# Optimization experiments

Hardware: AMD Instinct MI355X
Metric: run time of the kernel (lower is better)

## Reference

```python
import jax, jax.numpy as jnp
import numpy as np

# irrep blocks for 0e+1o+2e: dims 1, 3, 5 (total D=9)
BLOCKS = [(0, 1), (1, 4), (4, 9)]

def block_linear(x, W):
    # x: [N, C, 9], W: [3, C, C] -- e3nn Linear mixes channels within each irrep block
    outs = [jnp.einsum('ncd,cq->nqd', x[..., s:e], W[l]) for l, (s, e) in enumerate(BLOCKS)]
    return jnp.concatenate(outs, axis=-1)

def setup_inputs() -> dict:
    key = jax.random.key(0)
    ks = jax.random.split(key, 14)
    N, E, C, D, B, H, Z = 16384, 262144, 32, 9, 8, 64, 4
    inp = {
        'node_feats': jax.random.normal(ks[0], (N, C, D), jnp.float32),
        'node_attrs': jax.random.uniform(ks[1], (N, Z), jnp.float32),
        'edge_feats': jax.random.normal(ks[2], (E, B), jnp.float32),
        'edge_sh': jax.random.normal(ks[3], (E, D), jnp.float32),
        'cutoff': jax.random.uniform(ks[4], (E, 1), jnp.float32),
        # learned params
        'W_up': jax.random.normal(ks[5], (3, C, C), jnp.float32) / np.float32(np.sqrt(C)),
        'W1': jax.random.normal(ks[6], (B, H), jnp.float32) / np.float32(np.sqrt(B)),
        'W2': jax.random.normal(ks[7], (H, H), jnp.float32) / np.float32(np.sqrt(H)),
        'W3': jax.random.normal(ks[8], (H, C), jnp.float32) / np.float32(np.sqrt(H)),
        'W_lin': jax.random.normal(ks[9], (3, C, C), jnp.float32) / np.float32(np.sqrt(C)),
        'W_sc': jax.random.normal(ks[10], (Z, 3, C, C), jnp.float32) / np.float32(np.sqrt(C)),
        # fixed Clebsch-Gordan-like coupling tensor (constant structure of the TP)
        'CG': jax.random.normal(ks[11], (D, D, D), jnp.float32) / np.float32(D),
        'edge_src': jax.random.randint(ks[12], (E,), 0, N, jnp.int32),
        'edge_dst': jax.random.randint(ks[13], (E,), 0, N, jnp.int32),
    }
    return inp

def reference(node_feats, node_attrs, edge_feats, edge_sh, cutoff,
              W_up, W1, W2, W3, W_lin, W_sc, CG, edge_src, edge_dst):
    N = node_feats.shape[0]
    avg_num_neighbors = 16.0
    # linear_up: per-irrep channel mixing
    x = block_linear(node_feats, W_up)
    # radial MLP -> per-edge tensor-product weights, gated by cutoff
    h = jax.nn.silu(edge_feats @ W1)
    h = jax.nn.silu(h @ W2)
    w = (h @ W3) * cutoff  # [E, C]
    # gather source node feats, weighted equivariant tensor product per edge
    xs = x[edge_src]  # [E, C, D]
    m_ij = jnp.einsum('eci,ej,ijk,ec->eck', xs, edge_sh, CG, w)  # [E, C, D]
    # scatter-sum aggregation into destination nodes
    m_i = jax.ops.segment_sum(m_ij, edge_dst, num_segments=N)  # [N, C, D]
    # output linear + neighbor normalization
    m_i = block_linear(m_i, W_lin) / avg_num_neighbors
    # element-dependent self-connection from current message
    W_node = jnp.einsum('nz,zlcq->nlcq', node_attrs, W_sc)  # [N, 3, C, C]
    scs = jnp.concatenate(
        [jnp.einsum('ncd,ncq->nqd', m_i[..., s:e], W_node[:, l]) for l, (s, e) in enumerate(BLOCKS)],
        axis=-1)
    return (m_i, scs)
```

## Files before the change

### kernel.cpp

```cpp
#include <hip/hip_runtime.h>
#include <cstdint>

#define CC 32
#define DD 9
#define CD 288
#define BB 8
#define HH 64
#define ZZ 4
#define NB 8

typedef __attribute__((ext_vector_type(8))) short bf16x8;
typedef __attribute__((ext_vector_type(4))) float f32x4;
typedef __attribute__((ext_vector_type(2))) float f32x2;

__device__ __forceinline__ float silu_f(float v) {
  return v / (1.0f + __expf(-v));
}

__device__ __forceinline__ int blk_of(int d) { return d == 0 ? 0 : (d < 4 ? 1 : 2); }

__device__ __forceinline__ unsigned int f2bf(float f) {
  unsigned int u = __float_as_uint(f);
  return (u + 0x7fffu + ((u >> 16) & 1u)) >> 16;
}
__device__ __forceinline__ float bf_lo(unsigned int u) { return __uint_as_float(u << 16); }
__device__ __forceinline__ float bf_hi(unsigned int u) { return __uint_as_float(u & 0xffff0000u); }

__global__ __launch_bounds__(256) void k_zero(float* __restrict__ p, int n) {
  int i = blockIdx.x * 256 + threadIdx.x;
  if (i < n) p[i] = 0.0f;
}

__global__ __launch_bounds__(256) void k_hist(const int* __restrict__ edst,
                                              int* __restrict__ deg, int E) {
  int e = blockIdx.x * 256 + threadIdx.x;
  if (e < E) atomicAdd(&deg[edst[e]], 1);
}

__global__ __launch_bounds__(1024) void k_scan(const int* __restrict__ deg,
                                               int* __restrict__ offs,
                                               int* __restrict__ cursor, int N) {
  __shared__ int part[1024];
  int t = threadIdx.x;
  int chunk = (N + 1023) >> 10;
  int base = t * chunk;
  int lim = N - base; if (lim > chunk) lim = chunk; if (lim < 0) lim = 0;
  int s = 0;
  for (int i = 0; i < lim; ++i) s += deg[base + i];
  part[t] = s;
  __syncthreads();
  for (int off = 1; off < 1024; off <<= 1) {
    int v = part[t];
    int u = (t >= off) ? part[t - off] : 0;
    __syncthreads();
    part[t] = v + u;
    __syncthreads();
  }
  int run = (t == 0) ? 0 : part[t - 1];
  for (int i = 0; i < lim; ++i) {
    offs[base + i] = run;
    cursor[base + i] = run;
    run += deg[base + i];
  }
  if (t == 1023) offs[N] = run;
}

__global__ __launch_bounds__(256) void k_scatter(const int* __restrict__ edst,
                                                 const int* __restrict__ esrc,
                                                 const float* __restrict__ esh,
                                                 int* __restrict__ cursor,
                                                 int* __restrict__ eidx,
                                                 int* __restrict__ srcs,
                                                 unsigned int* __restrict__ esh_p, int E) {
  int e = blockIdx.x * 256 + threadIdx.x;
  if (e < E) {
    int d = edst[e];
    int pos = atomicAdd(&cursor[d], 1);
    eidx[pos] = e;
    srcs[pos] = esrc[e];
    const float* sp = esh + (size_t)e * 9;
    unsigned int* op = esh_p + (size_t)pos * 5;
#pragma unroll
    for (int jj = 0; jj < 5; ++jj) {
      unsigned int lo = f2bf(sp[2 * jj]);
      unsigned int hi = (jj < 4) ? f2bf(sp[2 * jj + 1]) : 0u;
      op[jj] = lo | (hi << 16);
    }
  }
}

__global__ __launch_bounds__(288, 1) void k_linear_up(
    const float* __restrict__ nf, const float* __restrict__ Wup,
    unsigned int* __restrict__ x_p, int N) {
  __shared__ float snf[NB][DD * 36];
  __shared__ float sval[NB][DD][CC];
  int t = threadIdx.x;
  int g = t >> 5, q = t & 31;
  int tc = t / 9, td = t - tc * 9;
  int l0 = blk_of(g);
  float wcol[CC];
#pragma unroll
  for (int c = 0; c < CC; ++c) wcol[c] = Wup[l0 * 1024 + c * 32 + q];
  int nbat = (N + NB - 1) / NB;
  int b = blockIdx.x;
  float r[NB];
  if (b < nbat) {
#pragma unroll
    for (int nb = 0; nb < NB; ++nb) {
      int n = b * NB + nb; if (n >= N) n = N - 1;
      r[nb] = nf[(size_t)n * CD + t];
    }
  }
  for (; b < nbat; b += gridDim.x) {
    int n0 = b * NB;
    __syncthreads();
#pragma unroll
    for (int nb = 0; nb < NB; ++nb) snf[nb][td * 36 + tc] = r[nb];
    __syncthreads();
    int b2 = b + gridDim.x;
    if (b2 < nbat) {
#pragma unroll
      for (int nb = 0; nb < NB; ++nb) {
        int n = b2 * NB + nb; if (n >= N) n = N - 1;
        r[nb] = nf[(size_t)n * CD + t];
      }
    }
#pragma unroll
    for (int nb = 0; nb < NB; ++nb) {
      const float4* rowp = (const float4*)(snf[nb] + g * 36);
      float a0 = 0.f, a1 = 0.f;
#pragma unroll
      for (int c4 = 0; c4 < 8; ++c4) {
        float4 bb = rowp[c4];
        a0 += bb.x * wcol[c4 * 4 + 0] + bb.y * wcol[c4 * 4 + 1];
        a1 += bb.z * wcol[c4 * 4 + 2] + bb.w * wcol[c4 * 4 + 3];
      }
      sval[nb][g][q] = a0 + a1;
    }
    __syncthreads();
#pragma unroll
    for (int it = 0; it < 5; ++it) {
      int idx = it * 288 + t;
      if (idx < NB * 160) {
        int nb = idx / 160, rr = idx - nb * 160;
        int p = rr >> 5, c = rr & 31;
        if (n0 + nb < N) {
          unsigned int lo = f2bf(sval[nb][2 * p][c]);
          unsigned int hi = (p < 4) ? f2bf(sval[nb][2 * p + 1][c]) : 0u;
          x_p[(size_t)(n0 + nb) * 160 + rr] = lo | (hi << 16);
        }
      }
    }
  }
}

__global__ __launch_bounds__(64) void k_mlp_mfma(
    const float* __restrict__ ef, const float* __restrict__ cut,
    const float* __restrict__ W1, const float* __restrict__ W2,
    const float* __restrict__ W3, const int* __restrict__ eidx,
    unsigned int* __restrict__ w_p, int E) {
  __shared__ ushort buf[4096];
  __shared__ float scut[64];
  int l = threadIdx.x;
  int h = l >> 4, li = l & 15;
  bf16x8 A2[4][2];
#pragma unroll
  for (int qm = 0; qm < 4; ++qm)
#pragma unroll
    for (int kb = 0; kb < 2; ++kb)
#pragma unroll
      for (int j = 0; j < 8; ++j)
        A2[qm][kb][j] = (short)f2bf(W2[(32 * kb + 8 * h + j) * HH + 16 * qm + li]);
  bf16x8 A3[2][2];
#pragma unroll
  for (int cm = 0; cm < 2; ++cm)
#pragma unroll
    for (int kb = 0; kb < 2; ++kb)
#pragma unroll
      for (int j = 0; j < 8; ++j)
        A3[cm][kb][j] = (short)f2bf(W3[(32 * kb + 8 * h + j) * CC + 16 * cm + li]);

  int ntile = E >> 6;
  for (int tile = blockIdx.x; tile < ntile; tile += gridDim.x) {
    int pos = tile * 64 + l;
    int eo = eidx[pos];
    const float4* efp = (const float4*)(ef + (size_t)eo * BB);
    float4 efa = efp[0];
    float4 efb = efp[1];
    scut[l] = cut[eo];
    float efv[BB] = {efa.x, efa.y, efa.z, efa.w, efb.x, efb.y, efb.z, efb.w};
#pragma unroll
    for (int g = 0; g < 8; ++g) {
      float hv[8];
#pragma unroll
      for (int jj = 0; jj < 8; ++jj) {
        int q = g * 8 + jj;
        float a = 0.f;
#pragma unroll
        for (int kin = 0; kin < BB; ++kin) a += efv[kin] * W1[kin * HH + q];
        hv[jj] = silu_f(a);
      }
      unsigned int d0 = f2bf(hv[0]) | (f2bf(hv[1]) << 16);
      unsigned int d1 = f2bf(hv[2]) | (f2bf(hv[3]) << 16);
      unsigned int d2 = f2bf(hv[4]) | (f2bf(hv[5]) << 16);
      unsigned int d3 = f2bf(hv[6]) | (f2bf(hv[7]) << 16);
      int F = ((l >> 4) * 2 + (g >> 2)) * 4 + (g & 3);
      *(uint4*)&buf[(F * 16 + li) * 8] = make_uint4(d0, d1, d2, d3);
    }
    f32x4 acc2[4][4];
#pragma unroll
    for (int qm = 0; qm < 4; ++qm)
#pragma unroll
      for (int nb = 0; nb < 4; ++nb) acc2[qm][nb] = (f32x4){0.f, 0.f, 0.f, 0.f};
#pragma unroll
    for (int nb = 0; nb < 4; ++nb)
#pragma unroll
      for (int kb = 0; kb < 2; ++kb) {
        int F = (nb * 2 + kb) * 4 + h;
        bf16x8 Bf = *(const bf16x8*)&buf[(F * 16 + li) * 8];
#pragma unroll
        for (int qm = 0; qm < 4; ++qm)
          acc2[qm][nb] = __builtin_amdgcn_mfma_f32_16x16x32_bf16(
              A2[qm][kb], Bf, acc2[qm][nb], 0, 0, 0);
      }
#pragma unroll
    for (int qm = 0; qm < 4; ++qm)
#pragma unroll
      for (int nb = 0; nb < 4; ++nb) {
        float v0 = silu_f(acc2[qm][nb][0]);
        float v1 = silu_f(acc2[qm][nb][1]);
        float v2 = silu_f(acc2[qm][nb][2]);
        float v3 = silu_f(acc2[qm][nb][3]);
        unsigned int lo = f2bf(v0) | (f2bf(v1) << 16);
        unsigned int hi = f2bf(v2) | (f2bf(v3) << 16);
        int G = (nb * 2 + (qm >> 1)) * 4 + ((2 * qm + (h >> 1)) & 3);
        *(uint2*)&buf[(G * 16 + li) * 8 + (h & 1) * 4] = make_uint2(lo, hi);
      }
    f32x4 acc3[2][4];
#pragma unroll
    for (int cm = 0; cm < 2; ++cm)
#pragma unroll
      for (int nb = 0; nb < 4; ++nb) acc3[cm][nb] = (f32x4){0.f, 0.f, 0.f, 0.f};
#pragma unroll
    for (int nb = 0; nb < 4; ++nb)
#pragma unroll
      for (int kb = 0; kb < 2; ++kb) {
        int G = (nb * 2 + kb) * 4 + h;
        bf16x8 Bf = *(const bf16x8*)&buf[(G * 16 + li) * 8];
#pragma unroll
        for (int cm = 0; cm < 2; ++cm)
          acc3[cm][nb] = __builtin_amdgcn_mfma_f32_16x16x32_bf16(
              A3[cm][kb], Bf, acc3[cm][nb], 0, 0, 0);
      }
#pragma unroll
    for (int nb = 0; nb < 4; ++nb) {
      float cv = scut[16 * nb + li];
#pragma unroll
      for (int cm = 0; cm < 2; ++cm) {
        unsigned int lo = f2bf(acc3[cm][nb][0] * cv) | (f2bf(acc3[cm][nb][1] * cv) << 16);
        unsigned int hi = f2bf(acc3[cm][nb][2] * cv) | (f2bf(acc3[cm][nb][3] * cv) << 16);
        *(uint2*)&w_p[(size_t)(tile * 64 + 16 * nb + li) * 16 + 8 * cm + 2 * h] =
            make_uint2(lo, hi);
      }
    }
  }
}

__global__ __launch_bounds__(256) void k_gather(
    const unsigned int* __restrict__ x_p, const unsigned int* __restrict__ w_p,
    const unsigned int* __restrict__ esh_p, const float* __restrict__ CG,
    const int* __restrict__ offs, const int* __restrict__ srcs,
    float* __restrict__ mpre, int N) {
  int wid = (blockIdx.x * 256 + threadIdx.x) >> 6;
  if (wid >= N) return;
  int lane = threadIdx.x & 63;
  int h = lane >> 5, c = lane & 31;
  int beg = offs[wid], end = offs[wid + 1];
  f32x2 Pp[36];
  float P8[9];
#pragma unroll
  for (int i = 0; i < 36; ++i) Pp[i] = (f32x2){0.f, 0.f};
#pragma unroll
  for (int i = 0; i < 9; ++i) P8[i] = 0.f;

  bool okc;
  unsigned int wu_c;
  unsigned int shd_c[5];
  unsigned int xd_c[5];
  {
    int p = beg + h;
    okc = p < end;
    int pp = okc ? p : beg;
    int s = srcs[pp];
    wu_c = w_p[(size_t)pp * 16 + (c >> 1)];
    const unsigned int* shp = esh_p + (size_t)pp * 5;
#pragma unroll
    for (int j = 0; j < 5; ++j) shd_c[j] = shp[j];
    const unsigned int* xp = x_p + (size_t)s * 160 + c;
    xd_c[0] = xp[0]; xd_c[1] = xp[32]; xd_c[2] = xp[64]; xd_c[3] = xp[96]; xd_c[4] = xp[128];
  }

  for (int p0 = beg; p0 < end; p0 += 2) {
    int pn = p0 + 2 + h;
    bool okn = pn < end;
    int ppn = okn ? pn : beg;
    int s_n = srcs[ppn];
    unsigned int wu_n = w_p[(size_t)ppn * 16 + (c >> 1)];
    unsigned int shd_n[5];
    {
      const unsigned int* shp = esh_p + (size_t)ppn * 5;
#pragma unroll
      for (int j = 0; j < 5; ++j) shd_n[j] = shp[j];
    }
    unsigned int xd_n[5];
    {
      const unsigned int* xp = x_p + (size_t)s_n * 160 + c;
      xd_n[0] = xp[0]; xd_n[1] = xp[32]; xd_n[2] = xp[64]; xd_n[3] = xp[96]; xd_n[4] = xp[128];
    }
    float wc = okc ? ((c & 1) ? bf_hi(wu_c) : bf_lo(wu_c)) : 0.f;
    f32x2 sh2[4];
    sh2[0] = (f32x2){bf_lo(shd_c[0]), bf_hi(shd_c[0])};
    sh2[1] = (f32x2){bf_lo(shd_c[1]), bf_hi(shd_c[1])};
    sh2[2] = (f32x2){bf_lo(shd_c[2]), bf_hi(shd_c[2])};
    sh2[3] = (f32x2){bf_lo(shd_c[3]), bf_hi(shd_c[3])};
    float sh8 = bf_lo(shd_c[4]);
    float xs[DD];
    xs[0] = bf_lo(xd_c[0]); xs[1] = bf_hi(xd_c[0]);
    xs[2] = bf_lo(xd_c[1]); xs[3] = bf_hi(xd_c[1]);
    xs[4] = bf_lo(xd_c[2]); xs[5] = bf_hi(xd_c[2]);
    xs[6] = bf_lo(xd_c[3]); xs[7] = bf_hi(xd_c[3]);
    xs[8] = bf_lo(xd_c[4]);
#pragma unroll
    for (int i = 0; i < DD; ++i) {
      float t = wc * xs[i];
      f32x2 t2 = (f32x2){t, t};
#pragma unroll
      for (int jp = 0; jp < 4; ++jp) Pp[i * 4 + jp] = t2 * sh2[jp] + Pp[i * 4 + jp];
      P8[i] += t * sh8;
    }
    okc = okn;
    wu_c = wu_n;
#pragma unroll
    for (int j = 0; j < 5; ++j) { shd_c[j] = shd_n[j]; xd_c[j] = xd_n[j]; }
  }

  f32x2 m2[4];
  float m8 = 0.f;
#pragma unroll
  for (int kp = 0; kp < 4; ++kp) m2[kp] = (f32x2){0.f, 0.f};
#pragma unroll
  for (int i = 0; i < DD; ++i) {
#pragma unroll
    for (int j = 0; j < DD; ++j) {
      float p = (j < 8) ? ((j & 1) ? Pp[i * 4 + (j >> 1)].y : Pp[i * 4 + (j >> 1)].x)
                        : P8[i];
      f32x2 p2 = (f32x2){p, p};
      const float* cgr = CG + i * 81 + j * DD;
#pragma unroll
      for (int kp = 0; kp < 4; ++kp) {
        f32x2 cg2 = (f32x2){cgr[2 * kp], cgr[2 * kp + 1]};
        m2[kp] = p2 * cg2 + m2[kp];
      }
      m8 += p * cgr[8];
    }
  }
  float m[DD];
  m[0] = m2[0].x; m[1] = m2[0].y;
  m[2] = m2[1].x; m[3] = m2[1].y;
  m[4] = m2[2].x; m[5] = m2[2].y;
  m[6] = m2[3].x; m[7] = m2[3].y;
  m[8] = m8;
#pragma unroll
  for (int k = 0; k < DD; ++k) m[k] += __shfl_xor(m[k], 32);
  if (h == 0) {
    float* mp = mpre + (size_t)wid * CD + c;
#pragma unroll
    for (int k = 0; k < DD; ++k) mp[k * 32] = m[k];
  }
}

__global__ __launch_bounds__(288, 1) void k_out(
    const float* __restrict__ attrs, const float* __restrict__ Wlin,
    const float* __restrict__ Wsc,
    float* __restrict__ out1, float* __restrict__ out2, int N) {
  __shared__ float smp[NB][CD];
  __shared__ float smt[NB][CD];
  __shared__ float sres1[NB * CD];
  __shared__ float sres2[NB * CD];
  int t = threadIdx.x;
  int g = t >> 5, q = t & 31;
  int l0 = blk_of(g);
  float wl[CC];
#pragma unroll
  for (int c = 0; c < CC; ++c) wl[c] = Wlin[l0 * 1024 + c * 32 + q];
  float ws0[CC], ws1[CC], ws2[CC], ws3[CC];
#pragma unroll
  for (int c = 0; c < CC; ++c) {
    ws0[c] = Wsc[0 * 3072 + l0 * 1024 + c * 32 + q];
    ws1[c] = Wsc[1 * 3072 + l0 * 1024 + c * 32 + q];
    ws2[c] = Wsc[2 * 3072 + l0 * 1024 + c * 32 + q];
    ws3[c] = Wsc[3 * 3072 + l0 * 1024 + c * 32 + q];
  }
  int nbat = (N + NB - 1) / NB;
  int b = blockIdx.x;
  float r[NB];
  if (b < nbat) {
#pragma unroll
    for (int nb = 0; nb < NB; ++nb) r[nb] = out2[(size_t)(b * NB + nb) * CD + t];
  }
  for (; b < nbat; b += gridDim.x) {
    int n0 = b * NB;
    __syncthreads();
#pragma unroll
    for (int nb = 0; nb < NB; ++nb) smp[nb][t] = r[nb];
    float4 av[NB];
#pragma unroll
    for (int nb = 0; nb < NB; ++nb) av[nb] = ((const float4*)attrs)[n0 + nb];
    __syncthreads();
    int b2 = b + gridDim.x;
    if (b2 < nbat) {
#pragma unroll
      for (int nb = 0; nb < NB; ++nb) r[nb] = out2[(size_t)(b2 * NB + nb) * CD + t];
    }
#pragma unroll
    for (int nb = 0; nb < NB; ++nb) {
      const float4* rowp = (const float4*)(smp[nb] + g * 32);
      float b0 = 0.f, b1 = 0.f;
#pragma unroll
      for (int c4 = 0; c4 < 8; ++c4) {
        float4 bb = rowp[c4];
        b0 += bb.x * wl[c4 * 4 + 0] + bb.y * wl[c4 * 4 + 1];
        b1 += bb.z * wl[c4 * 4 + 2] + bb.w * wl[c4 * 4 + 3];
      }
      float v = (b0 + b1) * (1.0f / 16.0f);
      smt[nb][t] = v;
      sres1[nb * CD + q * DD + g] = v;
    }
    __syncthreads();
#pragma unroll
    for (int nb = 0; nb < NB; ++nb) {
      const float4* rowp = (const float4*)(smt[nb] + g * 32);
      float z0 = 0.f, z1 = 0.f, z2 = 0.f, z3 = 0.f;
#pragma unroll
      for (int c4 = 0; c4 < 8; ++c4) {
        float4 bb = rowp[c4];
#pragma unroll
        for (int j = 0; j < 4; ++j) {
          float bv = (j == 0) ? bb.x : (j == 1) ? bb.y : (j == 2) ? bb.z : bb.w;
          int c = c4 * 4 + j;
          z0 += bv * ws0[c];
          z1 += bv * ws1[c];
          z2 += bv * ws2[c];
          z3 += bv * ws3[c];
        }
      }
      float4 a = av[nb];
      sres2[nb * CD + q * DD + g] = a.x * z0 + a.y * z1 + a.z * z2 + a.w * z3;
    }
    __syncthreads();
#pragma unroll
    for (int rr = 0; rr < (NB * 72) / 288; ++rr) {
      int s = rr * 288 + t;
      int nb = s / 72, idx = s - nb * 72;
      ((float4*)(out1 + (size_t)(n0 + nb) * CD))[idx] = ((const float4*)sres1)[s];
      ((float4*)(out2 + (size_t)(n0 + nb) * CD))[idx] = ((const float4*)sres2)[s];
    }
  }
}

extern "C" void kernel_launch(void* const* d_in, const int* in_sizes, int n_in,
                              void* d_out, int out_size, void* d_ws, size_t ws_size,
                              hipStream_t stream) {
  const float* nf    = (const float*)d_in[0];
  const float* attrs = (const float*)d_in[1];
  const float* ef    = (const float*)d_in[2];
  const float* esh   = (const float*)d_in[3];
  const float* cutv  = (const float*)d_in[4];
  const float* Wup   = (const float*)d_in[5];
  const float* W1    = (const float*)d_in[6];
  const float* W2    = (const float*)d_in[7];
  const float* W3    = (const float*)d_in[8];
  const float* Wlin  = (const float*)d_in[9];
  const float* Wsc   = (const float*)d_in[10];
  const float* CG    = (const float*)d_in[11];
  const int* esrc    = (const int*)d_in[12];
  const int* edst    = (const int*)d_in[13];
  int N = in_sizes[0] / CD;
  int E = in_sizes[12];
  float* out1 = (float*)d_out;
  float* out2 = out1 + (size_t)N * CD;

  unsigned int* x_p   = (unsigned int*)d_ws;
  unsigned int* w_p   = x_p + (size_t)N * 160;
  unsigned int* esh_p = w_p + (size_t)E * 16;
  int* deg     = (int*)(esh_p + (size_t)E * 5);
  int* offs    = deg + N;
  int* cursor  = offs + N + 1;
  int* eidx    = cursor + N;
  int* srcs    = eidx + E;

  k_zero<<<(N + 255) / 256, 256, 0, stream>>>((float*)deg, N);
  k_hist<<<(E + 255) / 256, 256, 0, stream>>>(edst, deg, E);
  k_scan<<<1, 1024, 0, stream>>>(deg, offs, cursor, N);
  k_scatter<<<(E + 255) / 256, 256, 0, stream>>>(edst, esrc, esh, cursor, eidx, srcs, esh_p, E);
  k_linear_up<<<512, 288, 0, stream>>>(nf, Wup, x_p, N);
  k_mlp_mfma<<<4096, 64, 0, stream>>>(ef, cutv, W1, W2, W3, eidx, w_p, E);
  k_gather<<<(N + 3) / 4, 256, 0, stream>>>(x_p, w_p, esh_p, CG, offs, srcs, out2, N);
  k_out<<<512, 288, 0, stream>>>(attrs, Wlin, Wsc, out1, out2, N);
}
```

Baseline: 236.5 us.

## Make gather kernel persistent with atomic work-stealing and cross-node prefetch

The gather kernel now launches a fixed grid of 2048 blocks. Each wavefront takes destination nodes from a global atomic counter, which is reset inside the scan kernel, instead of being given one node per wave. While it finishes the CG contraction for the current node, each wave prefetches the first edge data for the next node, so the load latency at node boundaries overlaps with compute. The aim is better load balance across nodes with uneven degree and fewer wave launch overheads. The cost is one atomic per node and a serialized dependency on the counter.

Result: slower. 478.8 us (+102.5%).

```diff
diff --git a/kernel.cpp b/kernel.cpp
--- a/kernel.cpp
+++ b/kernel.cpp
@@ -39,9 +39,11 @@
 
 __global__ __launch_bounds__(1024) void k_scan(const int* __restrict__ deg,
                                                int* __restrict__ offs,
-                                               int* __restrict__ cursor, int N) {
+                                               int* __restrict__ cursor,
+                                               int* __restrict__ wctr, int N) {
   __shared__ int part[1024];
   int t = threadIdx.x;
+  if (t == 0) wctr[0] = 0;
   int chunk = (N + 1023) >> 10;
   int base = t * chunk;
   int lim = N - base; if (lim > chunk) lim = chunk; if (lim < 0) lim = 0;
@@ -270,18 +272,18 @@
     const unsigned int* __restrict__ x_p, const unsigned int* __restrict__ w_p,
     const unsigned int* __restrict__ esh_p, const float* __restrict__ CG,
     const int* __restrict__ offs, const int* __restrict__ srcs,
-    float* __restrict__ mpre, int N) {
-  int wid = (blockIdx.x * 256 + threadIdx.x) >> 6;
-  if (wid >= N) return;
+    int* __restrict__ wctr, float* __restrict__ mpre, int N) {
   int lane = threadIdx.x & 63;
   int h = lane >> 5, c = lane & 31;
-  int beg = offs[wid], end = offs[wid + 1];
-  f32x2 Pp[36];
-  float P8[9];
-#pragma unroll
-  for (int i = 0; i < 36; ++i) Pp[i] = (f32x2){0.f, 0.f};
-#pragma unroll
-  for (int i = 0; i < 9; ++i) P8[i] = 0.f;
+
+  int cur;
+  {
+    int v = 0;
+    if (lane == 0) v = atomicAdd(wctr, 1);
+    cur = __shfl(v, 0, 64);
+  }
+  if (cur >= N) return;
+  int beg = offs[cur], end = offs[cur + 1];
 
   bool okc;
   unsigned int wu_c;
@@ -300,82 +302,116 @@
     xd_c[0] = xp[0]; xd_c[1] = xp[32]; xd_c[2] = xp[64]; xd_c[3] = xp[96]; xd_c[4] = xp[128];
   }
 
-  for (int p0 = beg; p0 < end; p0 += 2) {
-    int pn = p0 + 2 + h;
-    bool okn = pn < end;
-    int ppn = okn ? pn : beg;
-    int s_n = srcs[ppn];
-    unsigned int wu_n = w_p[(size_t)ppn * 16 + (c >> 1)];
-    unsigned int shd_n[5];
+  while (true) {
+    f32x2 Pp[36];
+    float P8[9];
+#pragma unroll
+    for (int i = 0; i < 36; ++i) Pp[i] = (f32x2){0.f, 0.f};
+#pragma unroll
+    for (int i = 0; i < 9; ++i) P8[i] = 0.f;
+
+    for (int p0 = beg; p0 < end; p0 += 2) {
+      int pn = p0 + 2 + h;
+      bool okn = pn < end;
+      int ppn = okn ? pn : beg;
+      int s_n = srcs[ppn];
+      unsigned int wu_n = w_p[(size_t)ppn * 16 + (c >> 1)];
+      unsigned int shd_n[5];
+      {
+        const unsigned int* shp = esh_p + (size_t)ppn * 5;
+#pragma unroll
+        for (int j = 0; j < 5; ++j) shd_n[j] = shp[j];
+      }
+      unsigned int xd_n[5];
+      {
+        const unsigned int* xp = x_p + (size_t)s_n * 160 + c;
+        xd_n[0] = xp[0]; xd_n[1] = xp[32]; xd_n[2] = xp[64]; xd_n[3] = xp[96]; xd_n[4] = xp[128];
+      }
+      float wc = okc ? ((c & 1) ? bf_hi(wu_c) : bf_lo(wu_c)) : 0.f;
+      f32x2 sh2[4];
+      sh2[0] = (f32x2){bf_lo(shd_c[0]), bf_hi(shd_c[0])};
+      sh2[1] = (f32x2){bf_lo(shd_c[1]), bf_hi(shd_c[1])};
+      sh2[2] = (f32x2){bf_lo(shd_c[2]), bf_hi(shd_c[2])};
+      sh2[3] = (f32x2){bf_lo(shd_c[3]), bf_hi(shd_c[3])};
+      float sh8 = bf_lo(shd_c[4]);
+      float xs[DD];
+      xs[0] = bf_lo(xd_c[0]); xs[1] = bf_hi(xd_c[0]);
+      xs[2] = bf_lo(xd_c[1]); xs[3] = bf_hi(xd_c[1]);
+      xs[4] = bf_lo(xd_c[2]); xs[5] = bf_hi(xd_c[2]);
+      xs[6] = bf_lo(xd_c[3]); xs[7] = bf_hi(xd_c[3]);
+      xs[8] = bf_lo(xd_c[4]);
+#pragma unroll
+      for (int i = 0; i < DD; ++i) {
+        float t = wc * xs[i];
+        f32x2 t2 = (f32x2){t, t};
+#pragma unroll
+        for (int jp = 0; jp < 4; ++jp) Pp[i * 4 + jp] = t2 * sh2[jp] + Pp[i * 4 + jp];
+        P8[i] += t * sh8;
+      }
+      okc = okn;
+      wu_c = wu_n;
+#pragma unroll
+      for (int j = 0; j < 5; ++j) { shd_c[j] = shd_n[j]; xd_c[j] = xd_n[j]; }
+    }
+
+    int nxt;
     {
-      const unsigned int* shp = esh_p + (size_t)ppn * 5;
-#pragma unroll
-      for (int j = 0; j < 5; ++j) shd_n[j] = shp[j];
-    }
-    unsigned int xd_n[5];
-    {
-      const unsigned int* xp = x_p + (size_t)s_n * 160 + c;
-      xd_n[0] = xp[0]; xd_n[1] = xp[32]; xd_n[2] = xp[64]; xd_n[3] = xp[96]; xd_n[4] = xp[128];
-    }
-    float wc = okc ? ((c & 1) ? bf_hi(wu_c) : bf_lo(wu_c)) : 0.f;
-    f32x2 sh2[4];
-    sh2[0] = (f32x2){bf_lo(shd_c[0]), bf_hi(shd_c[0])};
-    sh2[1] = (f32x2){bf_lo(shd_c[1]), bf_hi(shd_c[1])};
-    sh2[2] = (f32x2){bf_lo(shd_c[2]), bf_hi(shd_c[2])};
-    sh2[3] = (f32x2){bf_lo(shd_c[3]), bf_hi(shd_c[3])};
-    float sh8 = bf_lo(shd_c[4]);
-    float xs[DD];
-    xs[0] = bf_lo(xd_c[0]); xs[1] = bf_hi(xd_c[0]);
-    xs[2] = bf_lo(xd_c[1]); xs[3] = bf_hi(xd_c[1]);
-    xs[4] = bf_lo(xd_c[2]); xs[5] = bf_hi(xd_c[2]);
-    xs[6] = bf_lo(xd_c[3]); xs[7] = bf_hi(xd_c[3]);
-    xs[8] = bf_lo(xd_c[4]);
+      int v = 0;
+      if (lane == 0) v = atomicAdd(wctr, 1);
+      nxt = __shfl(v, 0, 64);
+    }
+    int beg_n = 0, end_n = 0;
+    if (nxt < N) {
+      beg_n = offs[nxt];
+      end_n = offs[nxt + 1];
+      int p = beg_n + h;
+      okc = p < end_n;
+      int pp = okc ? p : beg_n;
+      int s = srcs[pp];
+      wu_c = w_p[(size_t)pp * 16 + (c >> 1)];
+      const unsigned int* shp = esh_p + (size_t)pp * 5;
+#pragma unroll
+      for (int j = 0; j < 5; ++j) shd_c[j] = shp[j];
+      const unsigned int* xp = x_p + (size_t)s * 160 + c;
+      xd_c[0] = xp[0]; xd_c[1] = xp[32]; xd_c[2] = xp[64]; xd_c[3] = xp[96]; xd_c[4] = xp[128];
+    }
+
+    f32x2 m2[4];
+    float m8 = 0.f;
+#pragma unroll
+    for (int kp = 0; kp < 4; ++kp) m2[kp] = (f32x2){0.f, 0.f};
 #pragma unroll
     for (int i = 0; i < DD; ++i) {
-      float t = wc * xs[i];
-      f32x2 t2 = (f32x2){t, t};
-#pragma unroll
-      for (int jp = 0; jp < 4; ++jp) Pp[i * 4 + jp] = t2 * sh2[jp] + Pp[i * 4 + jp];
-      P8[i] += t * sh8;
-    }
-    okc = okn;
-    wu_c = wu_n;
-#pragma unroll
-    for (int j = 0; j < 5; ++j) { shd_c[j] = shd_n[j]; xd_c[j] = xd_n[j]; }
-  }
-
-  f32x2 m2[4];
-  float m8 = 0.f;
-#pragma unroll
-  for (int kp = 0; kp < 4; ++kp) m2[kp] = (f32x2){0.f, 0.f};
-#pragma unroll
-  for (int i = 0; i < DD; ++i) {
-#pragma unroll
-    for (int j = 0; j < DD; ++j) {
-      float p = (j < 8) ? ((j & 1) ? Pp[i * 4 + (j >> 1)].y : Pp[i * 4 + (j >> 1)].x)
-                        : P8[i];
-      f32x2 p2 = (f32x2){p, p};
-      const float* cgr = CG + i * 81 + j * DD;
-#pragma unroll
-      for (int kp = 0; kp < 4; ++kp) {
-        f32x2 cg2 = (f32x2){cgr[2 * kp], cgr[2 * kp + 1]};
-        m2[kp] = p2 * cg2 + m2[kp];
-      }
-      m8 += p * cgr[8];
-    }
-  }
-  float m[DD];
-  m[0] = m2[0].x; m[1] = m2[0].y;
-  m[2] = m2[1].x; m[3] = m2[1].y;
-  m[4] = m2[2].x; m[5] = m2[2].y;
-  m[6] = m2[3].x; m[7] = m2[3].y;
-  m[8] = m8;
-#pragma unroll
-  for (int k = 0; k < DD; ++k) m[k] += __shfl_xor(m[k], 32);
-  if (h == 0) {
-    float* mp = mpre + (size_t)wid * CD + c;
-#pragma unroll
-    for (int k = 0; k < DD; ++k) mp[k * 32] = m[k];
+#pragma unroll
+      for (int j = 0; j < DD; ++j) {
+        float p = (j < 8) ? ((j & 1) ? Pp[i * 4 + (j >> 1)].y : Pp[i * 4 + (j >> 1)].x)
+                          : P8[i];
+        f32x2 p2 = (f32x2){p, p};
+        const float* cgr = CG + i * 81 + j * DD;
+#pragma unroll
+        for (int kp = 0; kp < 4; ++kp) {
+          f32x2 cg2 = (f32x2){cgr[2 * kp], cgr[2 * kp + 1]};
+          m2[kp] = p2 * cg2 + m2[kp];
+        }
+        m8 += p * cgr[8];
+      }
+    }
+    float m[DD];
+    m[0] = m2[0].x; m[1] = m2[0].y;
+    m[2] = m2[1].x; m[3] = m2[1].y;
+    m[4] = m2[2].x; m[5] = m2[2].y;
+    m[6] = m2[3].x; m[7] = m2[3].y;
+    m[8] = m8;
+#pragma unroll
+    for (int k = 0; k < DD; ++k) m[k] += __shfl_xor(m[k], 32);
+    if (h == 0) {
+      float* mp = mpre + (size_t)cur * CD + c;
+#pragma unroll
+      for (int k = 0; k < DD; ++k) mp[k * 32] = m[k];
+    }
+
+    if (nxt >= N) break;
+    cur = nxt; beg = beg_n; end = end_n;
   }
 }
 
@@ -498,13 +534,14 @@
   int* cursor  = offs + N + 1;
   int* eidx    = cursor + N;
   int* srcs    = eidx + E;
+  int* wctr    = srcs + E;
 
   k_zero<<<(N + 255) / 256, 256, 0, stream>>>((float*)deg, N);
   k_hist<<<(E + 255) / 256, 256, 0, stream>>>(edst, deg, E);
-  k_scan<<<1, 1024, 0, stream>>>(deg, offs, cursor, N);
+  k_scan<<<1, 1024, 0, stream>>>(deg, offs, cursor, wctr, N);
   k_scatter<<<(E + 255) / 256, 256, 0, stream>>>(edst, esrc, esh, cursor, eidx, srcs, esh_p, E);
   k_linear_up<<<512, 288, 0, stream>>>(nf, Wup, x_p, N);
   k_mlp_mfma<<<4096, 64, 0, stream>>>(ef, cutv, W1, W2, W3, eidx, w_p, E);
-  k_gather<<<(N + 3) / 4, 256, 0, stream>>>(x_p, w_p, esh_p, CG, offs, srcs, out2, N);
+  k_gather<<<2048, 256, 0, stream>>>(x_p, w_p, esh_p, CG, offs, srcs, wctr, out2, N);
   k_out<<<512, 288, 0, stream>>>(attrs, Wlin, Wsc, out1, out2, N);
 }
```
